# Kernel optimization log

Measured on AMD Instinct MI355X. Metric: run time of the kernel, lower is better.

The kernel has to match this reference:

```python
import jax, jax.numpy as jnp
import numpy as np

D_MODEL = 1024
NUM_HEADS = 16
D_H = D_MODEL // NUM_HEADS
BATCH, SEQ = 4, 2048


def setup_inputs() -> dict:
    key = jax.random.key(0)
    kx, kq, kk, kv, ko = jax.random.split(key, 5)
    sigma = (2.0 / (D_MODEL + D_MODEL)) ** 0.5

    def trunc(k):
        return jax.random.truncated_normal(k, -3.0, 3.0, (D_MODEL, D_MODEL), dtype=jnp.float32) * sigma

    return {
        "x": jax.random.normal(kx, (BATCH, SEQ, D_MODEL), dtype=jnp.float32),
        "Wq": trunc(kq),
        "Wk": trunc(kk),
        "Wv": trunc(kv),
        "Wo": trunc(ko),
    }


def reference(x, Wq, Wk, Wv, Wo):
    B, S, D = x.shape
    H, Dh = NUM_HEADS, D_H
    # Linear: einsum('d_out d_in, ... d_in -> ... d_out')
    q = jnp.einsum('oi,bsi->bso', Wq, x)
    k = jnp.einsum('oi,bsi->bso', Wk, x)
    v = jnp.einsum('oi,bsi->bso', Wv, x)
    # split heads: [B, H, S, Dh]
    q = q.reshape(B, S, H, Dh).transpose(0, 2, 1, 3)
    k = k.reshape(B, S, H, Dh).transpose(0, 2, 1, 3)
    v = v.reshape(B, S, H, Dh).transpose(0, 2, 1, 3)
    scale = 1.0 / jnp.sqrt(jnp.asarray(Dh, dtype=x.dtype))
    score = jnp.einsum('bhnd,bhmd->bhnm', q, k) * scale  # [B,H,S,S]
    causal = jnp.tril(jnp.ones((S, S), dtype=bool))
    score = jnp.where(causal, score, -jnp.inf)
    attn = jax.nn.softmax(score, axis=-1)
    out = jnp.einsum('bhnm,bhmd->bhnd', attn, v)
    out = out.transpose(0, 2, 1, 3).reshape(B, S, D)
    return jnp.einsum('oi,bsi->bso', Wo, out)
```

## Files before the change

### kernel.cpp

```cpp
#include <hip/hip_runtime.h>
#include <hip/hip_bf16.h>

typedef __bf16 bf16x8 __attribute__((ext_vector_type(8)));
typedef __bf16 bf16x4 __attribute__((ext_vector_type(4)));
typedef float f32x4 __attribute__((ext_vector_type(4)));
typedef float f32x16 __attribute__((ext_vector_type(16)));

#define NB 4
#define NS 2048
#define ND 1024
#define NH 16
#define NDH 64
#define NM (NB*NS)

#define MFMA(a,b,c)   __builtin_amdgcn_mfma_f32_16x16x32_bf16((a),(b),(c),0,0,0)
#define MFMA32(a,b,c) __builtin_amdgcn_mfma_f32_32x32x16_bf16((a),(b),(c),0,0,0)

__device__ __forceinline__ void gload16(const void* g, void* l) {
    __builtin_amdgcn_global_load_lds(
        (const __attribute__((address_space(1))) void*)(g),
        (__attribute__((address_space(3))) void*)(l),
        16, 0, 0);
}

__device__ __forceinline__ unsigned cvt_pk_bf16(float lo, float hi) {
    unsigned w;
    asm("v_cvt_pk_bf16_f32 %0, %1, %2" : "=v"(w) : "v"(lo), "v"(hi));
    return w;
}
__device__ __forceinline__ float fmax3(float a, float b, float c) {
    float d;
    asm("v_max3_f32 %0, %1, %2, %3" : "=v"(d) : "v"(a), "v"(b), "v"(c));
    return d;
}
#define PLSWAP(a, b) asm("v_permlane32_swap_b32 %0, %1" : "+v"(a), "+v"(b))

__global__ __launch_bounds__(256) void cast4(const float* __restrict__ in,
                                             __bf16* __restrict__ out, int n) {
    int i = (blockIdx.x * 256 + threadIdx.x) * 4;
    if (i >= n) return;
    float4 v = *(const float4*)(in + i);
    bf16x4 o;
    o[0] = (__bf16)v.x; o[1] = (__bf16)v.y; o[2] = (__bf16)v.z; o[3] = (__bf16)v.w;
    *(bf16x4*)(out + i) = o;
}

__global__ __launch_bounds__(256) void cast4w(
    const float* __restrict__ w0, const float* __restrict__ w1,
    const float* __restrict__ w2, const float* __restrict__ w3,
    __bf16* __restrict__ o0, __bf16* __restrict__ o1,
    __bf16* __restrict__ o2, __bf16* __restrict__ o3) {
    const int z = blockIdx.y;
    const float* in  = (z == 0) ? w0 : (z == 1) ? w1 : (z == 2) ? w2 : w3;
    __bf16*      out = (z == 0) ? o0 : (z == 1) ? o1 : (z == 2) ? o2 : o3;
    int i = (blockIdx.x * 256 + threadIdx.x) * 4;
    float4 v = *(const float4*)(in + i);
    bf16x4 o;
    o[0] = (__bf16)v.x; o[1] = (__bf16)v.y; o[2] = (__bf16)v.z; o[3] = (__bf16)v.w;
    *(bf16x4*)(out + i) = o;
}

template<int MODE>
__global__ __launch_bounds__(256) void gemm128(
    const __bf16* __restrict__ A,
    const __bf16* __restrict__ W0, const __bf16* __restrict__ W1,
    const __bf16* __restrict__ W2,
    __bf16* __restrict__ O0, __bf16* __restrict__ O1, __bf16* __restrict__ O2,
    float* __restrict__ Cf)
{
    __shared__ alignas(16) __bf16 SB[2 * 128 * 32];
    __bf16* As = SB;
    __bf16* Bs = SB + 128 * 32;

    const int tid  = threadIdx.x;
    const int wave = tid >> 6, lane = tid & 63;
    const int l16  = lane & 15, lq = lane >> 4;
    const int bm = blockIdx.x * 128;
    const int bn = blockIdx.y * 128;
    const int z  = (MODE == 0) ? blockIdx.z : 0;
    const __bf16* __restrict__ Bw =
        (MODE == 0) ? ((z == 0) ? W0 : (z == 1) ? W1 : W2) : W0;

    const int wr = (wave >> 1) * 64;
    const int wc = (wave & 1) * 64;

    f32x4 acc[4][4];
    #pragma unroll
    for (int i = 0; i < 4; i++)
        #pragma unroll
        for (int j = 0; j < 4; j++)
            acc[i][j] = (f32x4){0.f, 0.f, 0.f, 0.f};

    const int ch0 = tid, ch1 = tid + 256;
    const int r0 = ch0 >> 2, c0 = (ch0 & 3) * 8;
    const int r1 = ch1 >> 2, c1 = (ch1 & 3) * 8;

    for (int k0 = 0; k0 < ND; k0 += 32) {
        __syncthreads();
        gload16(A  + (size_t)(bm + r0) * ND + k0 + c0, As + ch0 * 8);
        gload16(Bw + (size_t)(bn + r0) * ND + k0 + c0, Bs + ch0 * 8);
        gload16(A  + (size_t)(bm + r1) * ND + k0 + c1, As + ch1 * 8);
        gload16(Bw + (size_t)(bn + r1) * ND + k0 + c1, Bs + ch1 * 8);
        __syncthreads();

        bf16x8 af[4], bf[4];
        #pragma unroll
        for (int i = 0; i < 4; i++) {
            af[i] = *(const bf16x8*)(As + (wr + i*16 + l16) * 32 + lq * 8);
            bf[i] = *(const bf16x8*)(Bs + (wc + i*16 + l16) * 32 + lq * 8);
        }
        #pragma unroll
        for (int i = 0; i < 4; i++)
            #pragma unroll
            for (int j = 0; j < 4; j++)
                acc[i][j] = MFMA(af[i], bf[j], acc[i][j]);
    }

    if (MODE == 0 && z == 2) {
        __bf16* T = SB;
        const int TP = 136;
        #pragma unroll 1
        for (int c = 0; c < 4; ++c) {
            __syncthreads();
            #pragma unroll
            for (int j = 0; j < 4; j++) {
                if (((wc + j * 16) >> 5) != c) continue;
                #pragma unroll
                for (int i = 0; i < 4; i++)
                    #pragma unroll
                    for (int r = 0; r < 4; r++) {
                        int row = wr + i*16 + lq*4 + r;
                        int col = wc + j*16 + l16 - c*32;
                        T[col * TP + row] = (__bf16)acc[i][j][r];
                    }
            }
            __syncthreads();
            #pragma unroll
            for (int u2 = 0; u2 < 2; u2++) {
                int idx  = tid + u2 * 256;
                int trow = idx >> 4, tu = idx & 15;
                int gcol = bn + c*32 + trow;
                int gs   = bm + tu * 8;
                bf16x8 val = *(const bf16x8*)&T[trow * TP + tu * 8];
                int hh = gcol >> 6, dh = gcol & 63;
                *(bf16x8*)&O2[(((size_t)(gs >> 11) * NH + hh) * NDH + dh) * NS
                              + (gs & 2047)] = val;
            }
        }
        return;
    }

    #pragma unroll
    for (int i = 0; i < 4; i++) {
        #pragma unroll
        for (int j = 0; j < 4; j++) {
            #pragma unroll
            for (int r = 0; r < 4; r++) {
                int row = bm + wr + i*16 + lq*4 + r;
                int col = bn + wc + j*16 + l16;
                float v = acc[i][j][r];
                if (MODE == 1) {
                    Cf[(size_t)row * ND + col] = v;
                } else {
                    if (z == 0) v *= 0.1803368801111204f;
                    int b = row >> 11, s = row & 2047;
                    int h = col >> 6,  dh = col & 63;
                    __bf16* dst = (z == 0) ? O0 : O1;
                    dst[(((size_t)b*NH + h)*NS + s)*NDH + dh] = (__bf16)v;
                }
            }
        }
    }
}

__global__ __launch_bounds__(256) void attn_st(
    const __bf16* __restrict__ Q, const __bf16* __restrict__ K,
    const __bf16* __restrict__ Vt, __bf16* __restrict__ Oa)
{
    __shared__ alignas(16) __bf16 Ks[32*64];
    __shared__ alignas(16) __bf16 Vs[64*32];
    __shared__ float Fs[4][32];

    const int tid  = threadIdx.x;
    const int wave = tid >> 6, lane = tid & 63;
    const int qq   = lane & 31, hi = lane >> 5;

    const int bid = blockIdx.x;
    const int jg  = 15 - (bid >> 6);
    const int bh  = (bid & 7) * 8 + ((bid >> 3) & 7);
    const int j   = 4 * jg + wave;
    const int q0  = 32 * j;
    const int nt  = 4 * jg + 4;

    const int b = bh >> 4, h = bh & 15;
    const size_t qkb = (size_t)bh * NS * NDH;
    const size_t vbb = (size_t)bh * NDH * NS;
    float* Fw = Fs[wave];

    bf16x8 qf[4];
    {
        const __bf16* qr = Q + qkb + (size_t)(q0 + qq) * NDH + hi * 8;
        #pragma unroll
        for (int c = 0; c < 4; c++) qf[c] = *(const bf16x8*)(qr + c * 16);
    }

    f32x16 o0 = (f32x16)0.f, o1 = (f32x16)0.f;
    float mr = -__builtin_inff(), lsum = 0.f;

    const int kr = tid >> 3, ku = tid & 7;
    const int vd = tid >> 2, vu = tid & 3;
    const __bf16* ksrc = K  + qkb + (size_t)kr * NDH + (size_t)((ku ^ (kr & 7)) * 8);
    const __bf16* vsrc = Vt + vbb + (size_t)vd * NS  + (size_t)((vu ^ ((vd >> 1) & 3)) * 8);
    __bf16* kdst = Ks + tid * 8;
    __bf16* vdst = Vs + tid * 8;

    const int vsw = (qq >> 1) & 3;

    #pragma unroll 1
    for (int t = 0; t < nt; ++t) {
        __syncthreads();
        gload16(ksrc, kdst);
        gload16(vsrc, vdst);
        asm volatile("s_waitcnt vmcnt(0)" ::: "memory");
        __syncthreads();

        if (t <= j) {
            bf16x8 kf[4], vf[4];
            #pragma unroll
            for (int c = 0; c < 4; c++)
                kf[c] = *(const bf16x8*)(Ks + qq * 64 + ((2 * c + hi) ^ (qq & 7)) * 8);
            vf[0] = *(const bf16x8*)(Vs + qq * 32        + ((hi)     ^ vsw) * 8);
            vf[1] = *(const bf16x8*)(Vs + qq * 32        + ((2 + hi) ^ vsw) * 8);
            vf[2] = *(const bf16x8*)(Vs + (qq + 32) * 32 + ((hi)     ^ vsw) * 8);
            vf[3] = *(const bf16x8*)(Vs + (qq + 32) * 32 + ((2 + hi) ^ vsw) * 8);

            f32x16 s = (f32x16)0.f;
            __builtin_amdgcn_s_setprio(1);
            #pragma unroll
            for (int c = 0; c < 4; c++) s = MFMA32(kf[c], qf[c], s);
            __builtin_amdgcn_s_setprio(0);

            if (t == j) {
                #pragma unroll
                for (int r = 0; r < 16; r++) {
                    const int crow = (r & 3) + 8 * (r >> 2) + 4 * hi;
                    if (crow > qq) s[r] = -__builtin_inff();
                }
            }

            float a0 = fmax3(s[0],  s[1],  s[2]);
            float a1 = fmax3(s[3],  s[4],  s[5]);
            float a2 = fmax3(s[6],  s[7],  s[8]);
            float a3 = fmax3(s[9],  s[10], s[11]);
            float a4 = fmax3(s[12], s[13], s[14]);
            float tm = fmaxf(fmax3(a0, a1, a2), fmax3(a3, a4, s[15]));

            if (__any(tm > mr + 8.f)) {
                float rowm = fmaxf(tm, __shfl_xor(tm, 32));
                float mnew = fmaxf(mr, rowm);
                float fac  = exp2f(mr - mnew);
                mr = mnew; lsum *= fac;
                if (lane < 32) Fw[qq] = fac;
                f32x4 f0 = *(const f32x4*)&Fw[4 * hi];
                f32x4 f1 = *(const f32x4*)&Fw[8 + 4 * hi];
                f32x4 f2 = *(const f32x4*)&Fw[16 + 4 * hi];
                f32x4 f3 = *(const f32x4*)&Fw[24 + 4 * hi];
                #pragma unroll
                for (int i = 0; i < 4; i++) {
                    o0[i]      *= f0[i]; o1[i]      *= f0[i];
                    o0[4 + i]  *= f1[i]; o1[4 + i]  *= f1[i];
                    o0[8 + i]  *= f2[i]; o1[8 + i]  *= f2[i];
                    o0[12 + i] *= f3[i]; o1[12 + i] *= f3[i];
                }
            }

            float pv[16]; float psum = 0.f;
            #pragma unroll
            for (int r = 0; r < 16; r++) { pv[r] = exp2f(s[r] - mr); psum += pv[r]; }
            lsum += psum;

            unsigned w0 = cvt_pk_bf16(pv[0],  pv[1]);
            unsigned w1 = cvt_pk_bf16(pv[2],  pv[3]);
            unsigned w2 = cvt_pk_bf16(pv[4],  pv[5]);
            unsigned w3 = cvt_pk_bf16(pv[6],  pv[7]);
            unsigned w4 = cvt_pk_bf16(pv[8],  pv[9]);
            unsigned w5 = cvt_pk_bf16(pv[10], pv[11]);
            unsigned w6 = cvt_pk_bf16(pv[12], pv[13]);
            unsigned w7 = cvt_pk_bf16(pv[14], pv[15]);
            PLSWAP(w0, w2); PLSWAP(w1, w3);
            PLSWAP(w4, w6); PLSWAP(w5, w7);
            bf16x8 pa0 = __builtin_bit_cast(bf16x8, (uint4){w0, w1, w2, w3});
            bf16x8 pa1 = __builtin_bit_cast(bf16x8, (uint4){w4, w5, w6, w7});

            __builtin_amdgcn_s_setprio(1);
            o0 = MFMA32(pa0, vf[0], o0);
            o0 = MFMA32(pa1, vf[1], o0);
            o1 = MFMA32(pa0, vf[2], o1);
            o1 = MFMA32(pa1, vf[3], o1);
            __builtin_amdgcn_s_setprio(0);
        }

        ksrc += 32 * NDH;
        vsrc += 32;
    }

    lsum += __shfl_xor(lsum, 32);
    if (lane < 32) Fw[qq] = 1.f / lsum;
    f32x4 i0 = *(const f32x4*)&Fw[4 * hi];
    f32x4 i1 = *(const f32x4*)&Fw[8 + 4 * hi];
    f32x4 i2 = *(const f32x4*)&Fw[16 + 4 * hi];
    f32x4 i3 = *(const f32x4*)&Fw[24 + 4 * hi];
    __bf16* ob = Oa + ((size_t)b * NS + q0) * ND + h * 64 + qq;
    #pragma unroll
    for (int g2 = 0; g2 < 4; g2++) {
        f32x4 iv = (g2 == 0) ? i0 : (g2 == 1) ? i1 : (g2 == 2) ? i2 : i3;
        #pragma unroll
        for (int i = 0; i < 4; i++) {
            const int row = 8 * g2 + 4 * hi + i;
            ob[(size_t)row * ND]      = (__bf16)(o0[4 * g2 + i] * iv[i]);
            ob[(size_t)row * ND + 32] = (__bf16)(o1[4 * g2 + i] * iv[i]);
        }
    }
}

extern "C" void kernel_launch(void* const* d_in, const int* in_sizes, int n_in,
                              void* d_out, int out_size, void* d_ws, size_t ws_size,
                              hipStream_t stream) {
    const float* x  = (const float*)d_in[0];
    const float* wq = (const float*)d_in[1];
    const float* wk = (const float*)d_in[2];
    const float* wv = (const float*)d_in[3];
    const float* wo = (const float*)d_in[4];
    char* ws = (char*)d_ws;

    __bf16* xb  = (__bf16*)(ws);
    __bf16* wqb = (__bf16*)(ws + (16ull << 20));
    __bf16* wkb = (__bf16*)(ws + (18ull << 20));
    __bf16* wvb = (__bf16*)(ws + (20ull << 20));
    __bf16* wob = (__bf16*)(ws + (22ull << 20));
    __bf16* Qb  = (__bf16*)(ws + (24ull << 20));
    __bf16* Kb  = (__bf16*)(ws + (40ull << 20));
    __bf16* Vtb = (__bf16*)(ws + (56ull << 20));
    __bf16* Ab  = (__bf16*)(ws + (72ull << 20));
    float* out  = (float*)d_out;

    cast4<<<dim3(NM * ND / 1024), 256, 0, stream>>>(x, xb, NM * ND);
    cast4w<<<dim3(ND * ND / 1024, 4), 256, 0, stream>>>(
        wq, wk, wv, wo, wqb, wkb, wvb, wob);

    gemm128<0><<<dim3(NM/128, ND/128, 3), 256, 0, stream>>>(
        xb, wqb, wkb, wvb, Qb, Kb, Vtb, nullptr);

    attn_st<<<dim3(1024), 256, 0, stream>>>(Qb, Kb, Vtb, Ab);

    gemm128<1><<<dim3(NM/128, ND/128), 256, 0, stream>>>(
        Ab, wob, nullptr, nullptr, nullptr, nullptr, nullptr, out);
}
```

Before: 186.9 us.

## Load 64-key K/V tiles per barrier pair and reorder causal block schedule

The attention kernel now stages 64 keys of K and V per iteration instead of 32, processing two 32-key subtiles between each pair of barriers, which halves the number of synchronisations and global-load waits. The V tile layout changes to 64x64 with the same XOR swizzle as K. The block-to-query-group mapping is also permuted to interleave heavy and light causal workloads for better load balance. Shared memory use doubles, which may lower occupancy.

```diff
diff --git a/kernel.cpp b/kernel.cpp
--- a/kernel.cpp
+++ b/kernel.cpp
@@ -173,12 +173,12 @@
     }
 }
 
-__global__ __launch_bounds__(256) void attn_st(
+__global__ __launch_bounds__(256) void attn_st2(
     const __bf16* __restrict__ Q, const __bf16* __restrict__ K,
     const __bf16* __restrict__ Vt, __bf16* __restrict__ Oa)
 {
-    __shared__ alignas(16) __bf16 Ks[32*64];
-    __shared__ alignas(16) __bf16 Vs[64*32];
+    __shared__ alignas(16) __bf16 Ks[64*64];
+    __shared__ alignas(16) __bf16 Vs[64*64];
     __shared__ float Fs[4][32];
 
     const int tid  = threadIdx.x;
@@ -186,11 +186,12 @@
     const int qq   = lane & 31, hi = lane >> 5;
 
     const int bid = blockIdx.x;
-    const int jg  = 15 - (bid >> 6);
+    const int g   = bid >> 6;
+    const int jg  = ((g & 4) == 0) ? (15 - g) : ((g & 8) ? (g - 12) : (g + 4));
     const int bh  = (bid & 7) * 8 + ((bid >> 3) & 7);
     const int j   = 4 * jg + wave;
     const int q0  = 32 * j;
-    const int nt  = 4 * jg + 4;
+    const int nt  = 2 * jg + 2;
 
     const int b = bh >> 4, h = bh & 15;
     const size_t qkb = (size_t)bh * NS * NDH;
@@ -208,101 +209,104 @@
     float mr = -__builtin_inff(), lsum = 0.f;
 
     const int kr = tid >> 3, ku = tid & 7;
-    const int vd = tid >> 2, vu = tid & 3;
     const __bf16* ksrc = K  + qkb + (size_t)kr * NDH + (size_t)((ku ^ (kr & 7)) * 8);
-    const __bf16* vsrc = Vt + vbb + (size_t)vd * NS  + (size_t)((vu ^ ((vd >> 1) & 3)) * 8);
+    const __bf16* vsrc = Vt + vbb + (size_t)kr * NS  + (size_t)((ku ^ (kr & 7)) * 8);
     __bf16* kdst = Ks + tid * 8;
     __bf16* vdst = Vs + tid * 8;
 
-    const int vsw = (qq >> 1) & 3;
+#define SUBTILE(S, T)                                                         \
+    {                                                                         \
+        const int st = 2 * (T) + (S);                                         \
+        if (st <= j) {                                                        \
+            bf16x8 kf[4], vf[4];                                              \
+            _Pragma("unroll")                                                 \
+            for (int c = 0; c < 4; c++)                                       \
+                kf[c] = *(const bf16x8*)(Ks + (32*(S) + qq) * 64              \
+                                          + ((2*c + hi) ^ (qq & 7)) * 8);     \
+            vf[0] = *(const bf16x8*)(Vs + qq*64      + ((4*(S)+hi)   ^ (qq&7))*8); \
+            vf[1] = *(const bf16x8*)(Vs + qq*64      + ((4*(S)+2+hi) ^ (qq&7))*8); \
+            vf[2] = *(const bf16x8*)(Vs + (qq+32)*64 + ((4*(S)+hi)   ^ (qq&7))*8); \
+            vf[3] = *(const bf16x8*)(Vs + (qq+32)*64 + ((4*(S)+2+hi) ^ (qq&7))*8); \
+            f32x16 s = (f32x16)0.f;                                           \
+            __builtin_amdgcn_s_setprio(1);                                    \
+            _Pragma("unroll")                                                 \
+            for (int c = 0; c < 4; c++) s = MFMA32(kf[c], qf[c], s);          \
+            __builtin_amdgcn_s_setprio(0);                                    \
+            if (st == j) {                                                    \
+                _Pragma("unroll")                                             \
+                for (int r = 0; r < 16; r++) {                                \
+                    const int crow = (r & 3) + 8 * (r >> 2) + 4 * hi;         \
+                    if (crow > qq) s[r] = -__builtin_inff();                  \
+                }                                                             \
+            }                                                                 \
+            float a0 = fmax3(s[0],  s[1],  s[2]);                             \
+            float a1 = fmax3(s[3],  s[4],  s[5]);                             \
+            float a2 = fmax3(s[6],  s[7],  s[8]);                             \
+            float a3 = fmax3(s[9],  s[10], s[11]);                            \
+            float a4 = fmax3(s[12], s[13], s[14]);                            \
+            float tm = fmaxf(fmax3(a0, a1, a2), fmax3(a3, a4, s[15]));        \
+            if (__any(tm > mr + 8.f)) {                                       \
+                float rowm = fmaxf(tm, __shfl_xor(tm, 32));                   \
+                float mnew = fmaxf(mr, rowm);                                 \
+                float fac  = exp2f(mr - mnew);                                \
+                mr = mnew; lsum *= fac;                                       \
+                if (lane < 32) Fw[qq] = fac;                                  \
+                f32x4 f0 = *(const f32x4*)&Fw[4 * hi];                        \
+                f32x4 f1 = *(const f32x4*)&Fw[8 + 4 * hi];                    \
+                f32x4 f2 = *(const f32x4*)&Fw[16 + 4 * hi];                   \
+                f32x4 f3 = *(const f32x4*)&Fw[24 + 4 * hi];                   \
+                _Pragma("unroll")                                             \
+                for (int i = 0; i < 4; i++) {                                 \
+                    o0[i]      *= f0[i]; o1[i]      *= f0[i];                 \
+                    o0[4 + i]  *= f1[i]; o1[4 + i]  *= f1[i];                 \
+                    o0[8 + i]  *= f2[i]; o1[8 + i]  *= f2[i];                 \
+                    o0[12 + i] *= f3[i]; o1[12 + i] *= f3[i];                 \
+                }                                                             \
+            }                                                                 \
+            float pv[16]; float psum = 0.f;                                   \
+            _Pragma("unroll")                                                 \
+            for (int r = 0; r < 16; r++) {                                    \
+                pv[r] = exp2f(s[r] - mr); psum += pv[r];                      \
+            }                                                                 \
+            lsum += psum;                                                     \
+            unsigned w0 = cvt_pk_bf16(pv[0],  pv[1]);                         \
+            unsigned w1 = cvt_pk_bf16(pv[2],  pv[3]);                         \
+            unsigned w2 = cvt_pk_bf16(pv[4],  pv[5]);                         \
+            unsigned w3 = cvt_pk_bf16(pv[6],  pv[7]);                         \
+            unsigned w4 = cvt_pk_bf16(pv[8],  pv[9]);                         \
+            unsigned w5 = cvt_pk_bf16(pv[10], pv[11]);                        \
+            unsigned w6 = cvt_pk_bf16(pv[12], pv[13]);                        \
+            unsigned w7 = cvt_pk_bf16(pv[14], pv[15]);                        \
+            PLSWAP(w0, w2); PLSWAP(w1, w3);                                   \
+            PLSWAP(w4, w6); PLSWAP(w5, w7);                                   \
+            bf16x8 pa0 = __builtin_bit_cast(bf16x8, (uint4){w0, w1, w2, w3}); \
+            bf16x8 pa1 = __builtin_bit_cast(bf16x8, (uint4){w4, w5, w6, w7}); \
+            __builtin_amdgcn_s_setprio(1);                                    \
+            o0 = MFMA32(pa0, vf[0], o0);                                      \
+            o0 = MFMA32(pa1, vf[1], o0);                                      \
+            o1 = MFMA32(pa0, vf[2], o1);                                      \
+            o1 = MFMA32(pa1, vf[3], o1);                                      \
+            __builtin_amdgcn_s_setprio(0);                                    \
+        }                                                                     \
+    }
 
     #pragma unroll 1
     for (int t = 0; t < nt; ++t) {
         __syncthreads();
         gload16(ksrc, kdst);
+        gload16(ksrc + 32 * NDH, kdst + 2048);
         gload16(vsrc, vdst);
+        gload16(vsrc + 32 * NS, vdst + 2048);
         asm volatile("s_waitcnt vmcnt(0)" ::: "memory");
         __syncthreads();
 
-        if (t <= j) {
-            bf16x8 kf[4], vf[4];
-            #pragma unroll
-            for (int c = 0; c < 4; c++)
-                kf[c] = *(const bf16x8*)(Ks + qq * 64 + ((2 * c + hi) ^ (qq & 7)) * 8);
-            vf[0] = *(const bf16x8*)(Vs + qq * 32        + ((hi)     ^ vsw) * 8);
-            vf[1] = *(const bf16x8*)(Vs + qq * 32        + ((2 + hi) ^ vsw) * 8);
-            vf[2] = *(const bf16x8*)(Vs + (qq + 32) * 32 + ((hi)     ^ vsw) * 8);
-            vf[3] = *(const bf16x8*)(Vs + (qq + 32) * 32 + ((2 + hi) ^ vsw) * 8);
-
-            f32x16 s = (f32x16)0.f;
-            __builtin_amdgcn_s_setprio(1);
-            #pragma unroll
-            for (int c = 0; c < 4; c++) s = MFMA32(kf[c], qf[c], s);
-            __builtin_amdgcn_s_setprio(0);
-
-            if (t == j) {
-                #pragma unroll
-                for (int r = 0; r < 16; r++) {
-                    const int crow = (r & 3) + 8 * (r >> 2) + 4 * hi;
-                    if (crow > qq) s[r] = -__builtin_inff();
-                }
-            }
-
-            float a0 = fmax3(s[0],  s[1],  s[2]);
-            float a1 = fmax3(s[3],  s[4],  s[5]);
-            float a2 = fmax3(s[6],  s[7],  s[8]);
-            float a3 = fmax3(s[9],  s[10], s[11]);
-            float a4 = fmax3(s[12], s[13], s[14]);
-            float tm = fmaxf(fmax3(a0, a1, a2), fmax3(a3, a4, s[15]));
-
-            if (__any(tm > mr + 8.f)) {
-                float rowm = fmaxf(tm, __shfl_xor(tm, 32));
-                float mnew = fmaxf(mr, rowm);
-                float fac  = exp2f(mr - mnew);
-                mr = mnew; lsum *= fac;
-                if (lane < 32) Fw[qq] = fac;
-                f32x4 f0 = *(const f32x4*)&Fw[4 * hi];
-                f32x4 f1 = *(const f32x4*)&Fw[8 + 4 * hi];
-                f32x4 f2 = *(const f32x4*)&Fw[16 + 4 * hi];
-                f32x4 f3 = *(const f32x4*)&Fw[24 + 4 * hi];
-                #pragma unroll
-                for (int i = 0; i < 4; i++) {
-                    o0[i]      *= f0[i]; o1[i]      *= f0[i];
-                    o0[4 + i]  *= f1[i]; o1[4 + i]  *= f1[i];
-                    o0[8 + i]  *= f2[i]; o1[8 + i]  *= f2[i];
-                    o0[12 + i] *= f3[i]; o1[12 + i] *= f3[i];
-                }
-            }
-
-            float pv[16]; float psum = 0.f;
-            #pragma unroll
-            for (int r = 0; r < 16; r++) { pv[r] = exp2f(s[r] - mr); psum += pv[r]; }
-            lsum += psum;
-
-            unsigned w0 = cvt_pk_bf16(pv[0],  pv[1]);
-            unsigned w1 = cvt_pk_bf16(pv[2],  pv[3]);
-            unsigned w2 = cvt_pk_bf16(pv[4],  pv[5]);
-            unsigned w3 = cvt_pk_bf16(pv[6],  pv[7]);
-            unsigned w4 = cvt_pk_bf16(pv[8],  pv[9]);
-            unsigned w5 = cvt_pk_bf16(pv[10], pv[11]);
-            unsigned w6 = cvt_pk_bf16(pv[12], pv[13]);
-            unsigned w7 = cvt_pk_bf16(pv[14], pv[15]);
-            PLSWAP(w0, w2); PLSWAP(w1, w3);
-            PLSWAP(w4, w6); PLSWAP(w5, w7);
-            bf16x8 pa0 = __builtin_bit_cast(bf16x8, (uint4){w0, w1, w2, w3});
-            bf16x8 pa1 = __builtin_bit_cast(bf16x8, (uint4){w4, w5, w6, w7});
-
-            __builtin_amdgcn_s_setprio(1);
-            o0 = MFMA32(pa0, vf[0], o0);
-            o0 = MFMA32(pa1, vf[1], o0);
-            o1 = MFMA32(pa0, vf[2], o1);
-            o1 = MFMA32(pa1, vf[3], o1);
-            __builtin_amdgcn_s_setprio(0);
-        }
-
-        ksrc += 32 * NDH;
-        vsrc += 32;
-    }
+        SUBTILE(0, t)
+        SUBTILE(1, t)
+
+        ksrc += 64 * NDH;
+        vsrc += 64;
+    }
+#undef SUBTILE
 
     lsum += __shfl_xor(lsum, 32);
     if (lane < 32) Fw[qq] = 1.f / lsum;
@@ -351,7 +355,7 @@
     gemm128<0><<<dim3(NM/128, ND/128, 3), 256, 0, stream>>>(
         xb, wqb, wkb, wvb, Qb, Kb, Vtb, nullptr);
 
-    attn_st<<<dim3(1024), 256, 0, stream>>>(Qb, Kb, Vtb, Ab);
+    attn_st2<<<dim3(1024), 256, 0, stream>>>(Qb, Kb, Vtb, Ab);
 
     gemm128<1><<<dim3(NM/128, ND/128), 256, 0, stream>>>(
         Ab, wob, nullptr, nullptr, nullptr, nullptr, nullptr, out);
```

Result: no change. 188.4 us (+0.8%).

## Double-buffer K/V tiles in attention and reorder causal block scheduling

Applied to the files above, without the earlier changes.

The attention kernel now keeps two LDS buffers for K and V tiles. It prefetches the next tile with global_load_lds while computing on the current one, so the wait for loads to finish before each tile is removed. The mapping from block index to query-group is also changed to interleave heavy and light causal groups, aiming at better load balance. This doubles LDS use, which may affect occupancy, and relies on vmcnt accounting and raw s_barrier being correct.

```diff
diff --git a/kernel.cpp b/kernel.cpp
--- a/kernel.cpp
+++ b/kernel.cpp
@@ -173,12 +173,14 @@
     }
 }
 
-__global__ __launch_bounds__(256) void attn_st(
+__global__ __launch_bounds__(256) void attn_db(
     const __bf16* __restrict__ Q, const __bf16* __restrict__ K,
     const __bf16* __restrict__ Vt, __bf16* __restrict__ Oa)
 {
-    __shared__ alignas(16) __bf16 Ks[32*64];
-    __shared__ alignas(16) __bf16 Vs[64*32];
+    __shared__ alignas(16) __bf16 Ks0[32*64];
+    __shared__ alignas(16) __bf16 Ks1[32*64];
+    __shared__ alignas(16) __bf16 Vs0[64*32];
+    __shared__ alignas(16) __bf16 Vs1[64*32];
     __shared__ float Fs[4][32];
 
     const int tid  = threadIdx.x;
@@ -186,7 +188,8 @@
     const int qq   = lane & 31, hi = lane >> 5;
 
     const int bid = blockIdx.x;
-    const int jg  = 15 - (bid >> 6);
+    const int g   = bid >> 6;
+    const int jg  = ((g & 4) == 0) ? (15 - g) : ((g & 8) ? (g - 12) : (g + 4));
     const int bh  = (bid & 7) * 8 + ((bid >> 3) & 7);
     const int j   = 4 * jg + wave;
     const int q0  = 32 * j;
@@ -211,98 +214,106 @@
     const int vd = tid >> 2, vu = tid & 3;
     const __bf16* ksrc = K  + qkb + (size_t)kr * NDH + (size_t)((ku ^ (kr & 7)) * 8);
     const __bf16* vsrc = Vt + vbb + (size_t)vd * NS  + (size_t)((vu ^ ((vd >> 1) & 3)) * 8);
-    __bf16* kdst = Ks + tid * 8;
-    __bf16* vdst = Vs + tid * 8;
 
     const int vsw = (qq >> 1) & 3;
 
+#define COMPUTE(KS, VS, T)                                                    \
+    if ((T) <= j) {                                                           \
+        bf16x8 kf[4], vf[4];                                                  \
+        _Pragma("unroll")                                                     \
+        for (int c = 0; c < 4; c++)                                           \
+            kf[c] = *(const bf16x8*)((KS) + qq * 64 + ((2*c + hi) ^ (qq & 7)) * 8); \
+        vf[0] = *(const bf16x8*)((VS) + qq * 32        + ((hi)     ^ vsw) * 8);     \
+        vf[1] = *(const bf16x8*)((VS) + qq * 32        + ((2 + hi) ^ vsw) * 8);     \
+        vf[2] = *(const bf16x8*)((VS) + (qq + 32) * 32 + ((hi)     ^ vsw) * 8);     \
+        vf[3] = *(const bf16x8*)((VS) + (qq + 32) * 32 + ((2 + hi) ^ vsw) * 8);     \
+        f32x16 s = (f32x16)0.f;                                               \
+        __builtin_amdgcn_s_setprio(1);                                        \
+        _Pragma("unroll")                                                     \
+        for (int c = 0; c < 4; c++) s = MFMA32(kf[c], qf[c], s);              \
+        __builtin_amdgcn_s_setprio(0);                                        \
+        if ((T) == j) {                                                       \
+            _Pragma("unroll")                                                 \
+            for (int r = 0; r < 16; r++) {                                    \
+                const int crow = (r & 3) + 8 * (r >> 2) + 4 * hi;             \
+                if (crow > qq) s[r] = -__builtin_inff();                      \
+            }                                                                 \
+        }                                                                     \
+        float a0 = fmax3(s[0],  s[1],  s[2]);                                 \
+        float a1 = fmax3(s[3],  s[4],  s[5]);                                 \
+        float a2 = fmax3(s[6],  s[7],  s[8]);                                 \
+        float a3 = fmax3(s[9],  s[10], s[11]);                                \
+        float a4 = fmax3(s[12], s[13], s[14]);                                \
+        float tm = fmaxf(fmax3(a0, a1, a2), fmax3(a3, a4, s[15]));            \
+        if (__any(tm > mr + 8.f)) {                                           \
+            float rowm = fmaxf(tm, __shfl_xor(tm, 32));                       \
+            float mnew = fmaxf(mr, rowm);                                     \
+            float fac  = exp2f(mr - mnew);                                    \
+            mr = mnew; lsum *= fac;                                           \
+            if (lane < 32) Fw[qq] = fac;                                      \
+            f32x4 f0 = *(const f32x4*)&Fw[4 * hi];                            \
+            f32x4 f1 = *(const f32x4*)&Fw[8 + 4 * hi];                        \
+            f32x4 f2 = *(const f32x4*)&Fw[16 + 4 * hi];                       \
+            f32x4 f3 = *(const f32x4*)&Fw[24 + 4 * hi];                       \
+            _Pragma("unroll")                                                 \
+            for (int i = 0; i < 4; i++) {                                     \
+                o0[i]      *= f0[i]; o1[i]      *= f0[i];                     \
+                o0[4 + i]  *= f1[i]; o1[4 + i]  *= f1[i];                     \
+                o0[8 + i]  *= f2[i]; o1[8 + i]  *= f2[i];                     \
+                o0[12 + i] *= f3[i]; o1[12 + i] *= f3[i];                     \
+            }                                                                 \
+        }                                                                     \
+        float pv[16]; float psum = 0.f;                                       \
+        _Pragma("unroll")                                                     \
+        for (int r = 0; r < 16; r++) { pv[r] = exp2f(s[r] - mr); psum += pv[r]; } \
+        lsum += psum;                                                         \
+        unsigned w0 = cvt_pk_bf16(pv[0],  pv[1]);                             \
+        unsigned w1 = cvt_pk_bf16(pv[2],  pv[3]);                             \
+        unsigned w2 = cvt_pk_bf16(pv[4],  pv[5]);                             \
+        unsigned w3 = cvt_pk_bf16(pv[6],  pv[7]);                             \
+        unsigned w4 = cvt_pk_bf16(pv[8],  pv[9]);                             \
+        unsigned w5 = cvt_pk_bf16(pv[10], pv[11]);                            \
+        unsigned w6 = cvt_pk_bf16(pv[12], pv[13]);                            \
+        unsigned w7 = cvt_pk_bf16(pv[14], pv[15]);                            \
+        PLSWAP(w0, w2); PLSWAP(w1, w3);                                       \
+        PLSWAP(w4, w6); PLSWAP(w5, w7);                                       \
+        bf16x8 pa0 = __builtin_bit_cast(bf16x8, (uint4){w0, w1, w2, w3});     \
+        bf16x8 pa1 = __builtin_bit_cast(bf16x8, (uint4){w4, w5, w6, w7});     \
+        __builtin_amdgcn_s_setprio(1);                                        \
+        o0 = MFMA32(pa0, vf[0], o0);                                          \
+        o0 = MFMA32(pa1, vf[1], o0);                                          \
+        o1 = MFMA32(pa0, vf[2], o1);                                          \
+        o1 = MFMA32(pa1, vf[3], o1);                                          \
+        __builtin_amdgcn_s_setprio(0);                                        \
+    }
+
+    gload16(ksrc, Ks0 + tid * 8);
+    gload16(vsrc, Vs0 + tid * 8);
+    ksrc += 32 * NDH; vsrc += 32;
+
     #pragma unroll 1
-    for (int t = 0; t < nt; ++t) {
-        __syncthreads();
-        gload16(ksrc, kdst);
-        gload16(vsrc, vdst);
-        asm volatile("s_waitcnt vmcnt(0)" ::: "memory");
-        __syncthreads();
-
-        if (t <= j) {
-            bf16x8 kf[4], vf[4];
-            #pragma unroll
-            for (int c = 0; c < 4; c++)
-                kf[c] = *(const bf16x8*)(Ks + qq * 64 + ((2 * c + hi) ^ (qq & 7)) * 8);
-            vf[0] = *(const bf16x8*)(Vs + qq * 32        + ((hi)     ^ vsw) * 8);
-            vf[1] = *(const bf16x8*)(Vs + qq * 32        + ((2 + hi) ^ vsw) * 8);
-            vf[2] = *(const bf16x8*)(Vs + (qq + 32) * 32 + ((hi)     ^ vsw) * 8);
-            vf[3] = *(const bf16x8*)(Vs + (qq + 32) * 32 + ((2 + hi) ^ vsw) * 8);
-
-            f32x16 s = (f32x16)0.f;
-            __builtin_amdgcn_s_setprio(1);
-            #pragma unroll
-            for (int c = 0; c < 4; c++) s = MFMA32(kf[c], qf[c], s);
-            __builtin_amdgcn_s_setprio(0);
-
-            if (t == j) {
-                #pragma unroll
-                for (int r = 0; r < 16; r++) {
-                    const int crow = (r & 3) + 8 * (r >> 2) + 4 * hi;
-                    if (crow > qq) s[r] = -__builtin_inff();
-                }
-            }
-
-            float a0 = fmax3(s[0],  s[1],  s[2]);
-            float a1 = fmax3(s[3],  s[4],  s[5]);
-            float a2 = fmax3(s[6],  s[7],  s[8]);
-            float a3 = fmax3(s[9],  s[10], s[11]);
-            float a4 = fmax3(s[12], s[13], s[14]);
-            float tm = fmaxf(fmax3(a0, a1, a2), fmax3(a3, a4, s[15]));
-
-            if (__any(tm > mr + 8.f)) {
-                float rowm = fmaxf(tm, __shfl_xor(tm, 32));
-                float mnew = fmaxf(mr, rowm);
-                float fac  = exp2f(mr - mnew);
-                mr = mnew; lsum *= fac;
-                if (lane < 32) Fw[qq] = fac;
-                f32x4 f0 = *(const f32x4*)&Fw[4 * hi];
-                f32x4 f1 = *(const f32x4*)&Fw[8 + 4 * hi];
-                f32x4 f2 = *(const f32x4*)&Fw[16 + 4 * hi];
-                f32x4 f3 = *(const f32x4*)&Fw[24 + 4 * hi];
-                #pragma unroll
-                for (int i = 0; i < 4; i++) {
-                    o0[i]      *= f0[i]; o1[i]      *= f0[i];
-                    o0[4 + i]  *= f1[i]; o1[4 + i]  *= f1[i];
-                    o0[8 + i]  *= f2[i]; o1[8 + i]  *= f2[i];
-                    o0[12 + i] *= f3[i]; o1[12 + i] *= f3[i];
-                }
-            }
-
-            float pv[16]; float psum = 0.f;
-            #pragma unroll
-            for (int r = 0; r < 16; r++) { pv[r] = exp2f(s[r] - mr); psum += pv[r]; }
-            lsum += psum;
-
-            unsigned w0 = cvt_pk_bf16(pv[0],  pv[1]);
-            unsigned w1 = cvt_pk_bf16(pv[2],  pv[3]);
-            unsigned w2 = cvt_pk_bf16(pv[4],  pv[5]);
-            unsigned w3 = cvt_pk_bf16(pv[6],  pv[7]);
-            unsigned w4 = cvt_pk_bf16(pv[8],  pv[9]);
-            unsigned w5 = cvt_pk_bf16(pv[10], pv[11]);
-            unsigned w6 = cvt_pk_bf16(pv[12], pv[13]);
-            unsigned w7 = cvt_pk_bf16(pv[14], pv[15]);
-            PLSWAP(w0, w2); PLSWAP(w1, w3);
-            PLSWAP(w4, w6); PLSWAP(w5, w7);
-            bf16x8 pa0 = __builtin_bit_cast(bf16x8, (uint4){w0, w1, w2, w3});
-            bf16x8 pa1 = __builtin_bit_cast(bf16x8, (uint4){w4, w5, w6, w7});
-
-            __builtin_amdgcn_s_setprio(1);
-            o0 = MFMA32(pa0, vf[0], o0);
-            o0 = MFMA32(pa1, vf[1], o0);
-            o1 = MFMA32(pa0, vf[2], o1);
-            o1 = MFMA32(pa1, vf[3], o1);
-            __builtin_amdgcn_s_setprio(0);
-        }
-
-        ksrc += 32 * NDH;
-        vsrc += 32;
-    }
+    for (int t = 0; t < nt; t += 2) {
+        gload16(ksrc, Ks1 + tid * 8);
+        gload16(vsrc, Vs1 + tid * 8);
+        ksrc += 32 * NDH; vsrc += 32;
+        asm volatile("s_waitcnt vmcnt(2)" ::: "memory");
+        __builtin_amdgcn_s_barrier();
+        COMPUTE(Ks0, Vs0, t)
+        __builtin_amdgcn_s_barrier();
+
+        if (t + 2 < nt) {
+            gload16(ksrc, Ks0 + tid * 8);
+            gload16(vsrc, Vs0 + tid * 8);
+            ksrc += 32 * NDH; vsrc += 32;
+            asm volatile("s_waitcnt vmcnt(2)" ::: "memory");
+        } else {
+            asm volatile("s_waitcnt vmcnt(0)" ::: "memory");
+        }
+        __builtin_amdgcn_s_barrier();
+        COMPUTE(Ks1, Vs1, t + 1)
+        __builtin_amdgcn_s_barrier();
+    }
+#undef COMPUTE
 
     lsum += __shfl_xor(lsum, 32);
     if (lane < 32) Fw[qq] = 1.f / lsum;
@@ -351,7 +362,7 @@
     gemm128<0><<<dim3(NM/128, ND/128, 3), 256, 0, stream>>>(
         xb, wqb, wkb, wvb, Qb, Kb, Vtb, nullptr);
 
-    attn_st<<<dim3(1024), 256, 0, stream>>>(Qb, Kb, Vtb, Ab);
+    attn_db<<<dim3(1024), 256, 0, stream>>>(Qb, Kb, Vtb, Ab);
 
     gemm128<1><<<dim3(NM/128, ND/128), 256, 0, stream>>>(
         Ab, wob, nullptr, nullptr, nullptr, nullptr, nullptr, out);
```

Result: no change. 186.9 us (+0.0%).

## Rewrite projection GEMMs as 8-wave double-buffered 128x256 tiles with swizzled LDS

Applied to the files above, without the earlier changes.

Replaces the 4-wave 128x128 GEMM (K step 32, single buffer, two syncs per step) with an 8-wave 128x256 tile, a K step of 64, and double-buffered LDS. The next stage's global-to-LDS loads are issued ahead and waited on with explicit vmcnt counts, so memory transfer overlaps the MFMA work. LDS chunks are XOR-swizzled to avoid bank conflicts, and s_setprio raises wave priority around the MFMA bursts. In exchange the kernel uses much more LDS and launches fewer blocks, which lowers occupancy and grid parallelism. The V-transpose epilogue is adapted to the wider tile.

```diff
diff --git a/kernel.cpp b/kernel.cpp
--- a/kernel.cpp
+++ b/kernel.cpp
@@ -61,28 +61,29 @@
 }
 
 template<int MODE>
-__global__ __launch_bounds__(256) void gemm128(
+__global__ __launch_bounds__(512) void gemm8p(
     const __bf16* __restrict__ A,
     const __bf16* __restrict__ W0, const __bf16* __restrict__ W1,
     const __bf16* __restrict__ W2,
     __bf16* __restrict__ O0, __bf16* __restrict__ O1, __bf16* __restrict__ O2,
     float* __restrict__ Cf)
 {
-    __shared__ alignas(16) __bf16 SB[2 * 128 * 32];
-    __bf16* As = SB;
-    __bf16* Bs = SB + 128 * 32;
+    __shared__ alignas(16) __bf16 As0[128*64];
+    __shared__ alignas(16) __bf16 As1[128*64];
+    __shared__ alignas(16) __bf16 Bs0[256*64];
+    __shared__ alignas(16) __bf16 Bs1[256*64];
 
     const int tid  = threadIdx.x;
     const int wave = tid >> 6, lane = tid & 63;
     const int l16  = lane & 15, lq = lane >> 4;
     const int bm = blockIdx.x * 128;
-    const int bn = blockIdx.y * 128;
+    const int bn = blockIdx.y * 256;
     const int z  = (MODE == 0) ? blockIdx.z : 0;
     const __bf16* __restrict__ Bw =
         (MODE == 0) ? ((z == 0) ? W0 : (z == 1) ? W1 : W2) : W0;
 
-    const int wr = (wave >> 1) * 64;
-    const int wc = (wave & 1) * 64;
+    const int wr = (wave >> 2) * 64;
+    const int wc = (wave & 3) * 64;
 
     f32x4 acc[4][4];
     #pragma unroll
@@ -91,36 +92,77 @@
         for (int j = 0; j < 4; j++)
             acc[i][j] = (f32x4){0.f, 0.f, 0.f, 0.f};
 
-    const int ch0 = tid, ch1 = tid + 256;
-    const int r0 = ch0 >> 2, c0 = (ch0 & 3) * 8;
-    const int r1 = ch1 >> 2, c1 = (ch1 & 3) * 8;
-
-    for (int k0 = 0; k0 < ND; k0 += 32) {
-        __syncthreads();
-        gload16(A  + (size_t)(bm + r0) * ND + k0 + c0, As + ch0 * 8);
-        gload16(Bw + (size_t)(bn + r0) * ND + k0 + c0, Bs + ch0 * 8);
-        gload16(A  + (size_t)(bm + r1) * ND + k0 + c1, As + ch1 * 8);
-        gload16(Bw + (size_t)(bn + r1) * ND + k0 + c1, Bs + ch1 * 8);
-        __syncthreads();
-
-        bf16x8 af[4], bf[4];
-        #pragma unroll
-        for (int i = 0; i < 4; i++) {
-            af[i] = *(const bf16x8*)(As + (wr + i*16 + l16) * 32 + lq * 8);
-            bf[i] = *(const bf16x8*)(Bs + (wc + i*16 + l16) * 32 + lq * 8);
-        }
-        #pragma unroll
-        for (int i = 0; i < 4; i++)
-            #pragma unroll
-            for (int j = 0; j < 4; j++)
-                acc[i][j] = MFMA(af[i], bf[j], acc[i][j]);
-    }
+    const int arow = tid >> 3;
+    const int au   = (tid & 7) ^ (arow & 7);
+    const __bf16* Ag0 = A  + (size_t)(bm + arow) * ND + au * 8;
+    const __bf16* Ag1 = Ag0 + (size_t)64 * ND;
+    const __bf16* Bg0 = Bw + (size_t)(bn + arow) * ND + au * 8;
+    const __bf16* Bg1 = Bg0 + (size_t)64 * ND;
+    const __bf16* Bg2 = Bg0 + (size_t)128 * ND;
+    const __bf16* Bg3 = Bg0 + (size_t)192 * ND;
+
+#define STAGE(AS, BS, K0)                                  \
+    {                                                      \
+        gload16(Ag0 + (K0), (AS) + tid * 8);               \
+        gload16(Ag1 + (K0), (AS) + (tid + 512) * 8);       \
+        gload16(Bg0 + (K0), (BS) + tid * 8);               \
+        gload16(Bg1 + (K0), (BS) + (tid + 512) * 8);       \
+        gload16(Bg2 + (K0), (BS) + (tid + 1024) * 8);      \
+        gload16(Bg3 + (K0), (BS) + (tid + 1536) * 8);      \
+    }
+
+    const int asw = l16 & 7;
+
+#define PHASE(AS, BS, KK)                                                     \
+    {                                                                         \
+        bf16x8 af[4], bfr[4];                                                 \
+        _Pragma("unroll")                                                     \
+        for (int i = 0; i < 4; i++)                                           \
+            af[i] = *(const bf16x8*)((AS) + (wr + i*16 + l16) * 64            \
+                                      + (((KK)*4 + lq) ^ asw) * 8);           \
+        _Pragma("unroll")                                                     \
+        for (int j = 0; j < 4; j++)                                           \
+            bfr[j] = *(const bf16x8*)((BS) + (wc + j*16 + l16) * 64           \
+                                       + (((KK)*4 + lq) ^ asw) * 8);          \
+        __builtin_amdgcn_s_setprio(1);                                        \
+        _Pragma("unroll")                                                     \
+        for (int i = 0; i < 4; i++)                                           \
+            _Pragma("unroll")                                                 \
+            for (int j = 0; j < 4; j++)                                       \
+                acc[i][j] = MFMA(af[i], bfr[j], acc[i][j]);                   \
+        __builtin_amdgcn_s_setprio(0);                                        \
+    }
+
+    STAGE(As0, Bs0, 0)
+
+    #pragma unroll 1
+    for (int t = 0; t < 16; t += 2) {
+        if (t + 1 < 16) STAGE(As1, Bs1, (t + 1) * 64)
+        if (t + 1 < 16) { asm volatile("s_waitcnt vmcnt(6)" ::: "memory"); }
+        else            { asm volatile("s_waitcnt vmcnt(0)" ::: "memory"); }
+        __builtin_amdgcn_s_barrier();
+        PHASE(As0, Bs0, 0)
+        __builtin_amdgcn_s_barrier();
+        PHASE(As0, Bs0, 1)
+        __builtin_amdgcn_s_barrier();
+
+        if (t + 2 < 16) STAGE(As0, Bs0, (t + 2) * 64)
+        if (t + 2 < 16) { asm volatile("s_waitcnt vmcnt(6)" ::: "memory"); }
+        else            { asm volatile("s_waitcnt vmcnt(0)" ::: "memory"); }
+        __builtin_amdgcn_s_barrier();
+        PHASE(As1, Bs1, 0)
+        __builtin_amdgcn_s_barrier();
+        PHASE(As1, Bs1, 1)
+        __builtin_amdgcn_s_barrier();
+    }
+#undef STAGE
+#undef PHASE
 
     if (MODE == 0 && z == 2) {
-        __bf16* T = SB;
+        __bf16* T = As0;
         const int TP = 136;
         #pragma unroll 1
-        for (int c = 0; c < 4; ++c) {
+        for (int c = 0; c < 8; ++c) {
             __syncthreads();
             #pragma unroll
             for (int j = 0; j < 4; j++) {
@@ -135,10 +177,8 @@
                     }
             }
             __syncthreads();
-            #pragma unroll
-            for (int u2 = 0; u2 < 2; u2++) {
-                int idx  = tid + u2 * 256;
-                int trow = idx >> 4, tu = idx & 15;
+            {
+                int trow = tid >> 4, tu = tid & 15;
                 int gcol = bn + c*32 + trow;
                 int gs   = bm + tu * 8;
                 bf16x8 val = *(const bf16x8*)&T[trow * TP + tu * 8];
@@ -348,11 +388,11 @@
     cast4w<<<dim3(ND * ND / 1024, 4), 256, 0, stream>>>(
         wq, wk, wv, wo, wqb, wkb, wvb, wob);
 
-    gemm128<0><<<dim3(NM/128, ND/128, 3), 256, 0, stream>>>(
+    gemm8p<0><<<dim3(NM/128, ND/256, 3), 512, 0, stream>>>(
         xb, wqb, wkb, wvb, Qb, Kb, Vtb, nullptr);
 
     attn_st<<<dim3(1024), 256, 0, stream>>>(Qb, Kb, Vtb, Ab);
 
-    gemm128<1><<<dim3(NM/128, ND/128), 256, 0, stream>>>(
+    gemm8p<1><<<dim3(NM/128, ND/256), 512, 0, stream>>>(
         Ab, wob, nullptr, nullptr, nullptr, nullptr, nullptr, out);
 }
```

Measured after the change: 186.3 us. Within noise of the previous version (-0.3%).
